# Performance work log

Hardware: AMD Instinct MI355X
Metric: run time of the kernel (lower is better)

The kernel has to match this reference:

```python
import jax, jax.numpy as jnp
import numpy as np

ITERATIONS = 3
EPS = 1e-06

def squash(s):
    # square_norm along last dim, keepdims (matches torch squash)
    sq = jnp.sum(s * s, axis=-1, keepdims=True)
    return sq / (1.0 + sq) * s / (jnp.sqrt(sq) + EPS)

def setup_inputs() -> dict:
    key = jax.random.key(0)
    k1, k2 = jax.random.split(key)
    x = jax.random.normal(k1, (64, 32, 8, 8, 16), dtype=jnp.float32)
    W = jax.random.normal(k2, (1, 32, 8, 8, 32, 16, 32), dtype=jnp.float32)
    return {"x": x, "W": W}

def reference(x, W):
    # u_hat: (B, C, H, Wd, O, D) = x (B,C,H,Wd,I) @ W (C,H,Wd,O,I,D)
    u_hat = jnp.einsum('bchwi,chwoid->bchwod', x, W[0])
    b = jnp.zeros(u_hat.shape[:-1], dtype=u_hat.dtype)  # (B,C,H,Wd,O)
    for _ in range(ITERATIONS - 1):
        c = jax.nn.softmax(b, axis=-1)
        s = jnp.sum(c[..., None] * u_hat, axis=(1, 2, 3))  # (B,O,D)
        v = squash(s)
        b = b + jnp.sum(u_hat * v[:, None, None, None], axis=-1)
    c = jax.nn.softmax(b, axis=-1)
    s = jnp.sum(c[..., None] * u_hat, axis=(1, 2, 3))
    return squash(s)  # (B, out_capsules, out_cap_dim)
```

## Files before the change

### kernel.cpp

```cpp
#include <hip/hip_runtime.h>
#include <math.h>

#define B_ 64
#define N_ 2048
#define O_ 32
#define I_ 16
#define D_ 32
#define OD_ 1024

typedef __attribute__((ext_vector_type(8))) short bf16x8;
typedef __attribute__((ext_vector_type(4))) float f32x4;

union FragU { unsigned u[4]; uint4 v; bf16x8 f; };

__device__ __forceinline__ void barrier_lds() {
  asm volatile("s_waitcnt lgkmcnt(0)\n\ts_barrier" ::: "memory");
}

template <int CTRL>
__device__ __forceinline__ float dpp_mov_f(float x) {
  return __int_as_float(
      __builtin_amdgcn_update_dpp(0, __float_as_int(x), CTRL, 0xf, 0xf, true));
}
__device__ __forceinline__ float row16_sum(float x) {
  x += dpp_mov_f<0x128>(x);
  x += dpp_mov_f<0x124>(x);
  x += dpp_mov_f<0x4e>(x);
  x += dpp_mov_f<0xb1>(x);
  return x;
}
__device__ __forceinline__ float grp32_max(float x) {
  x = fmaxf(x, dpp_mov_f<0xb1>(x));
  x = fmaxf(x, dpp_mov_f<0x4e>(x));
  x = fmaxf(x, dpp_mov_f<0x124>(x));
  x = fmaxf(x, dpp_mov_f<0x128>(x));
  x = fmaxf(x, __shfl_xor(x, 16));
  return x;
}
__device__ __forceinline__ float grp32_sum(float x) {
  x += dpp_mov_f<0xb1>(x);
  x += dpp_mov_f<0x4e>(x);
  x += dpp_mov_f<0x124>(x);
  x += dpp_mov_f<0x128>(x);
  x += __shfl_xor(x, 16);
  return x;
}

__device__ __forceinline__ void dk_split(float f, unsigned &h, unsigned &l) {
  unsigned u = __float_as_uint(f);
  h = u & 0xffff0000u;
  float lo = f - __uint_as_float(h);
  l = __float_as_uint(lo) >> 16;
}
__device__ __forceinline__ void dk_split16(float f, unsigned short &h,
                                           unsigned short &l) {
  unsigned u = __float_as_uint(f);
  unsigned hu = u & 0xffff0000u;
  h = (unsigned short)(u >> 16);
  float lo = f - __uint_as_float(hu);
  l = (unsigned short)(__float_as_uint(lo) >> 16);
}
__device__ __forceinline__ unsigned pk(unsigned short e0, unsigned short e1) {
  return (unsigned)e0 | ((unsigned)e1 << 16);
}

__global__ __launch_bounds__(256) void prep_all(const float* __restrict__ W,
                                                const float* __restrict__ x,
                                                uint4* __restrict__ WP,
                                                uint4* __restrict__ XP) {
  __shared__ float tile[8 * 512];
  const int tid = threadIdx.x;
  if (blockIdx.x < 8192) {
    const int pair0 = blockIdx.x * 8;
    const float4* gsrc = (const float4*)(W + (size_t)pair0 * 512);
    float4* lds4 = (float4*)tile;
#pragma unroll
    for (int k = 0; k < 4; ++k) lds4[tid + k * 256] = gsrc[tid + k * 256];
    __syncthreads();
    const int p = tid >> 5;
    const int d = tid & 31;
    const int pair = pair0 + p;
    unsigned short hh[I_], ll[I_];
#pragma unroll
    for (int i = 0; i < I_; ++i)
      dk_split16(tile[p * 512 + i * 32 + d], hh[i], ll[i]);
    const int c = d & 15, dhalf = d >> 4;
    size_t base = ((size_t)pair * 2 + dhalf) * 4;
#pragma unroll
    for (int sel = 0; sel < 2; ++sel) {
      const unsigned short* e = sel ? ll : hh;
#pragma unroll
      for (int qp = 0; qp < 2; ++qp) {
        uint4 u;
        u.x = pk(e[qp * 8 + 0], e[qp * 8 + 1]);
        u.y = pk(e[qp * 8 + 2], e[qp * 8 + 3]);
        u.z = pk(e[qp * 8 + 4], e[qp * 8 + 5]);
        u.w = pk(e[qp * 8 + 6], e[qp * 8 + 7]);
        WP[(base + sel * 2 + qp) * 16 + c] = u;
      }
    }
  } else {
    int t = (blockIdx.x - 8192) * 256 + tid;
    int c = t & 15, n = (t >> 4) & 2047, bg = t >> 15;
    const float4* xq =
        (const float4*)(x + ((size_t)(bg * 16 + c) * N_ + n) * I_);
    float xv[I_];
#pragma unroll
    for (int k = 0; k < 4; ++k) {
      float4 q4 = xq[k];
      xv[4 * k + 0] = q4.x;
      xv[4 * k + 1] = q4.y;
      xv[4 * k + 2] = q4.z;
      xv[4 * k + 3] = q4.w;
    }
    unsigned short hh[I_], ll[I_];
#pragma unroll
    for (int i = 0; i < I_; ++i) dk_split16(xv[i], hh[i], ll[i]);
    size_t base = ((size_t)bg * N_ + n) * 4;
#pragma unroll
    for (int sel = 0; sel < 2; ++sel) {
      const unsigned short* e = sel ? ll : hh;
#pragma unroll
      for (int qp = 0; qp < 2; ++qp) {
        uint4 u;
        u.x = pk(e[qp * 8 + 0], e[qp * 8 + 1]);
        u.y = pk(e[qp * 8 + 2], e[qp * 8 + 3]);
        u.z = pk(e[qp * 8 + 4], e[qp * 8 + 5]);
        u.w = pk(e[qp * 8 + 6], e[qp * 8 + 7]);
        XP[(base + sel * 2 + qp) * 16 + c] = u;
      }
    }
  }
}

template <int UNIFORM>
__global__ __launch_bounds__(1024, 4) void mfma_pass6(
    const uint4* __restrict__ XP, const uint4* __restrict__ WP,
    const float* __restrict__ v, float* __restrict__ partial, int NC) {
  const int tid = threadIdx.x;
  const int lane = tid & 63;
  const int w = tid >> 6;
  const int q = lane >> 4;
  const int c = lane & 15;
  const int qp = q & 1;
  const int ch = blockIdx.x;
  const int bgy = blockIdx.y;

  __shared__ uint4 xps[2][16][4][16];
  __shared__ float ls_logit[32 * O_];
  __shared__ float ls_c[32 * O_];

  const int n0 = ch * NC;

  {
    uint4* xf = (uint4*)xps;
    const int total = 2 * NC * 64;
    for (int l = tid; l < total; l += 1024) {
      int bgl = l / (NC * 64);
      int rest = l - bgl * (NC * 64);
      xf[bgl * 1024 + rest] =
          XP[(size_t)(bgy * 2 + bgl) * 131072 + (size_t)n0 * 64 + rest];
    }
  }

  f32x4 s_t[2][4];
#pragma unroll
  for (int bgl = 0; bgl < 2; ++bgl)
#pragma unroll
    for (int ct = 0; ct < 4; ++ct) s_t[bgl][ct] = (f32x4){0.f, 0.f, 0.f, 0.f};

  float vreg[2][4][4];
  if (!UNIFORM) {
#pragma unroll
    for (int bgl = 0; bgl < 2; ++bgl)
#pragma unroll
      for (int ct = 0; ct < 4; ++ct) {
        int odc = (2 * w + (ct >> 1)) * 32 + (ct & 1) * 16 + c;
#pragma unroll
        for (int r = 0; r < 4; ++r)
          vreg[bgl][ct][r] =
              v[(size_t)(bgy * 32 + bgl * 16 + q * 4 + r) * OD_ + odc];
      }
  }

  barrier_lds();

  const uint4* wbase = WP + (size_t)(2 * w) * 128 + lane;

  for (int nl = 0; nl < NC; ++nl) {
    const size_t n = (size_t)(n0 + nl);

    FragU cb[4];
#pragma unroll
    for (int ct = 0; ct < 4; ++ct) cb[ct].v = wbase[n * 4096 + ct * 64];

    if (UNIFORM) {
#pragma unroll
      for (int bgl = 0; bgl < 2; ++bgl) {
        FragU ah, al;
        ah.v = xps[bgl][nl][qp][c];
        al.v = xps[bgl][nl][2 + qp][c];
#pragma unroll
        for (int ct = 0; ct < 4; ++ct) {
          s_t[bgl][ct] = __builtin_amdgcn_mfma_f32_16x16x32_bf16(
              ah.f, cb[ct].f, s_t[bgl][ct], 0, 0, 0);
          s_t[bgl][ct] = __builtin_amdgcn_mfma_f32_16x16x32_bf16(
              al.f, cb[ct].f, s_t[bgl][ct], 0, 0, 0);
        }
      }
    } else {
      float lg[2][2][4];
#pragma unroll
      for (int bgl = 0; bgl < 2; ++bgl)
#pragma unroll
        for (int ol = 0; ol < 2; ++ol)
#pragma unroll
          for (int r = 0; r < 4; ++r) lg[bgl][ol][r] = 0.f;
#pragma unroll
      for (int bgl = 0; bgl < 2; ++bgl) {
        FragU ah, al;
        ah.v = xps[bgl][nl][qp][c];
        al.v = xps[bgl][nl][2 + qp][c];
#pragma unroll
        for (int ct = 0; ct < 4; ++ct) {
          f32x4 acc = (f32x4){0.f, 0.f, 0.f, 0.f};
          acc = __builtin_amdgcn_mfma_f32_16x16x32_bf16(ah.f, cb[ct].f, acc, 0, 0, 0);
          f32x4 u = __builtin_amdgcn_mfma_f32_16x16x32_bf16(al.f, cb[ct].f, acc, 0, 0, 0);
          int ol = ct >> 1;
#pragma unroll
          for (int r = 0; r < 4; ++r)
            lg[bgl][ol][r] = fmaf(u[r], vreg[bgl][ct][r], lg[bgl][ol][r]);
        }
      }
#pragma unroll
      for (int bgl = 0; bgl < 2; ++bgl)
#pragma unroll
        for (int ol = 0; ol < 2; ++ol)
#pragma unroll
          for (int r = 0; r < 4; ++r) lg[bgl][ol][r] = row16_sum(lg[bgl][ol][r]);
      if (c == 0) {
#pragma unroll
        for (int bgl = 0; bgl < 2; ++bgl)
#pragma unroll
          for (int ol = 0; ol < 2; ++ol)
#pragma unroll
            for (int r = 0; r < 4; ++r)
              ls_logit[(bgl * 16 + q * 4 + r) * O_ + 2 * w + ol] = lg[bgl][ol][r];
      }
      barrier_lds();
      {
        float l = ls_logit[tid];
        float mx = grp32_max(l);
        float e = __expf(l - mx);
        float sm = grp32_sum(e);
        ls_c[tid] = e / sm;
      }
      barrier_lds();
#pragma unroll
      for (int bgl = 0; bgl < 2; ++bgl) {
        FragU ah, al;
        ah.v = xps[bgl][nl][qp][c];
        al.v = xps[bgl][nl][2 + qp][c];
#pragma unroll
        for (int ct = 0; ct < 4; ++ct) {
          f32x4 acc = (f32x4){0.f, 0.f, 0.f, 0.f};
          acc = __builtin_amdgcn_mfma_f32_16x16x32_bf16(ah.f, cb[ct].f, acc, 0, 0, 0);
          f32x4 u = __builtin_amdgcn_mfma_f32_16x16x32_bf16(al.f, cb[ct].f, acc, 0, 0, 0);
          int o = 2 * w + (ct >> 1);
#pragma unroll
          for (int r = 0; r < 4; ++r) {
            float cc = ls_c[(bgl * 16 + q * 4 + r) * O_ + o];
            s_t[bgl][ct][r] = fmaf(cc, u[r], s_t[bgl][ct][r]);
          }
        }
      }
    }
  }

  const float scale = UNIFORM ? (1.f / 32.f) : 1.f;
#pragma unroll
  for (int bgl = 0; bgl < 2; ++bgl)
#pragma unroll
    for (int ct = 0; ct < 4; ++ct) {
      int odc = (2 * w + (ct >> 1)) * 32 + (ct & 1) * 16 + c;
#pragma unroll
      for (int r = 0; r < 4; ++r) {
        partial[((size_t)ch * B_ + bgy * 32 + bgl * 16 + q * 4 + r) * OD_ + odc] =
            s_t[bgl][ct][r] * scale;
      }
    }
}

template <int UNIFORM>
__global__ __launch_bounds__(512, 4) void mfma_pass_fb(
    const float* __restrict__ x, const float* __restrict__ W,
    const float* __restrict__ v, float* __restrict__ partial, int NC) {
  const int tid = threadIdx.x;
  const int lane = tid & 63;
  const int cg = tid >> 6;
  const int q = lane >> 4;
  const int c = lane & 15;
  const int ch = blockIdx.x;
  const int bg = blockIdx.y;

  __shared__ float ls_logit[16 * O_];
  __shared__ float ls_c[16 * O_];

  f32x4 s_t[8];
#pragma unroll
  for (int ct = 0; ct < 8; ++ct) s_t[ct] = (f32x4){0.f, 0.f, 0.f, 0.f};

  const int n0 = ch * NC;
  const int ih = (q & 1) * 8;
  const float* xrow = x + ((size_t)(bg * 16 + c) * N_) * I_ + ih;

  for (int nl = 0; nl < NC; ++nl) {
    const int n = n0 + nl;
    const float* xp = xrow + (size_t)n * I_;
    float4 xv0 = *(const float4*)xp;
    float4 xv1 = *(const float4*)(xp + 4);
    float xv[8] = {xv0.x, xv0.y, xv0.z, xv0.w, xv1.x, xv1.y, xv1.z, xv1.w};
    FragU a1;
#pragma unroll
    for (int p = 0; p < 4; ++p) {
      unsigned h0, l0, h1, l1;
      dk_split(xv[2 * p], h0, l0);
      dk_split(xv[2 * p + 1], h1, l1);
      a1.u[p] = (q < 2) ? ((h0 >> 16) | h1) : (l0 | (l1 << 16));
    }
    f32x4 u_t[8];
#pragma unroll
    for (int ct = 0; ct < 8; ++ct) {
      const int o = cg * 4 + (ct >> 1);
      const int d = (ct & 1) * 16 + c;
      const float* wp = W + (((size_t)n * O_ + o) * I_ + ih) * D_ + d;
      FragU b1, b2;
#pragma unroll
      for (int p = 0; p < 4; ++p) {
        unsigned h0, l0, h1, l1;
        dk_split(wp[(2 * p) * D_], h0, l0);
        dk_split(wp[(2 * p + 1) * D_], h1, l1);
        b1.u[p] = (h0 >> 16) | h1;
        b2.u[p] = l0 | (l1 << 16);
      }
      if (UNIFORM) {
        s_t[ct] = __builtin_amdgcn_mfma_f32_16x16x32_bf16(a1.f, b1.f, s_t[ct], 0, 0, 0);
        s_t[ct] = __builtin_amdgcn_mfma_f32_16x16x32_bf16(a1.f, b2.f, s_t[ct], 0, 0, 0);
      } else {
        f32x4 acc = (f32x4){0.f, 0.f, 0.f, 0.f};
        acc = __builtin_amdgcn_mfma_f32_16x16x32_bf16(a1.f, b1.f, acc, 0, 0, 0);
        u_t[ct] = __builtin_amdgcn_mfma_f32_16x16x32_bf16(a1.f, b2.f, acc, 0, 0, 0);
      }
    }
    if (!UNIFORM) {
#pragma unroll
      for (int ol = 0; ol < 4; ++ol) {
        float lg[4] = {0.f, 0.f, 0.f, 0.f};
#pragma unroll
        for (int hf = 0; hf < 2; ++hf) {
          int ct = ol * 2 + hf;
          int odc = cg * 128 + ct * 16 + c;
#pragma unroll
          for (int r = 0; r < 4; ++r)
            lg[r] = fmaf(u_t[ct][r], v[(size_t)(bg * 16 + q * 4 + r) * OD_ + odc], lg[r]);
        }
#pragma unroll
        for (int r = 0; r < 4; ++r) {
#pragma unroll
          for (int m = 1; m < 16; m <<= 1) lg[r] += __shfl_xor(lg[r], m);
        }
        if (c == 0) {
#pragma unroll
          for (int r = 0; r < 4; ++r)
            ls_logit[(q * 4 + r) * O_ + cg * 4 + ol] = lg[r];
        }
      }
      __syncthreads();
      {
        int b_l = tid >> 5, o = tid & 31;
        float l = ls_logit[b_l * O_ + o];
        float mx = l;
#pragma unroll
        for (int m = 16; m >= 1; m >>= 1) mx = fmaxf(mx, __shfl_xor(mx, m));
        float e = __expf(l - mx);
        float sm = e;
#pragma unroll
        for (int m = 16; m >= 1; m >>= 1) sm += __shfl_xor(sm, m);
        ls_c[b_l * O_ + o] = e / sm;
      }
      __syncthreads();
#pragma unroll
      for (int ol = 0; ol < 4; ++ol) {
        int o = cg * 4 + ol;
        float cc[4];
#pragma unroll
        for (int r = 0; r < 4; ++r) cc[r] = ls_c[(q * 4 + r) * O_ + o];
#pragma unroll
        for (int hf = 0; hf < 2; ++hf) {
          int ct = ol * 2 + hf;
#pragma unroll
          for (int r = 0; r < 4; ++r)
            s_t[ct][r] = fmaf(cc[r], u_t[ct][r], s_t[ct][r]);
        }
      }
    }
  }

  const float scale = UNIFORM ? (1.f / 32.f) : 1.f;
#pragma unroll
  for (int ct = 0; ct < 8; ++ct) {
#pragma unroll
    for (int r = 0; r < 4; ++r) {
      partial[((size_t)ch * B_ + bg * 16 + q * 4 + r) * OD_ + cg * 128 + ct * 16 + c] =
          s_t[ct][r] * scale;
    }
  }
}

__global__ __launch_bounds__(256) void reduce_stageA(float4* __restrict__ part,
                                                     int cq) {
  int qa = blockIdx.x >> 6;
  int g4 = (blockIdx.x & 63) * 256 + threadIdx.x;
  float4 s = make_float4(0.f, 0.f, 0.f, 0.f);
  for (int i = 0; i < cq; ++i) {
    float4 p = part[(size_t)(qa * cq + i) * 16384 + g4];
    s.x += p.x; s.y += p.y; s.z += p.z; s.w += p.w;
  }
  part[(size_t)(qa * cq) * 16384 + g4] = s;
}

__global__ __launch_bounds__(256) void reduce_stageB(
    const float4* __restrict__ part, int cq, const float4* __restrict__ prev,
    float4* __restrict__ out) {
  int g4 = blockIdx.x * 256 + threadIdx.x;
  float4 s = make_float4(0.f, 0.f, 0.f, 0.f);
#pragma unroll
  for (int qa = 0; qa < 4; ++qa) {
    float4 p = part[(size_t)(qa * cq) * 16384 + g4];
    s.x += p.x; s.y += p.y; s.z += p.z; s.w += p.w;
  }
  float sq = s.x * s.x + s.y * s.y + s.z * s.z + s.w * s.w;
#pragma unroll
  for (int m = 4; m >= 1; m >>= 1) sq += __shfl_xor(sq, m, 8);
  float scale = sq / ((1.f + sq) * (sqrtf(sq) + 1e-6f));
  float4 r = make_float4(s.x * scale, s.y * scale, s.z * scale, s.w * scale);
  if (prev) {
    float4 p = prev[g4];
    r.x += p.x; r.y += p.y; r.z += p.z; r.w += p.w;
  }
  out[g4] = r;
}

__global__ __launch_bounds__(256) void reduce_squash(
    const float4* __restrict__ part, int chunks,
    const float4* __restrict__ prev, float4* __restrict__ out) {
  int g4 = blockIdx.x * 256 + threadIdx.x;
  float4 s = make_float4(0.f, 0.f, 0.f, 0.f);
#pragma unroll 4
  for (int ch = 0; ch < chunks; ++ch) {
    float4 p = part[(size_t)ch * 16384 + g4];
    s.x += p.x; s.y += p.y; s.z += p.z; s.w += p.w;
  }
  float sq = s.x * s.x + s.y * s.y + s.z * s.z + s.w * s.w;
#pragma unroll
  for (int m = 4; m >= 1; m >>= 1) sq += __shfl_xor(sq, m, 8);
  float scale = sq / ((1.f + sq) * (sqrtf(sq) + 1e-6f));
  float4 r = make_float4(s.x * scale, s.y * scale, s.z * scale, s.w * scale);
  if (prev) {
    float4 p = prev[g4];
    r.x += p.x; r.y += p.y; r.z += p.z; r.w += p.w;
  }
  out[g4] = r;
}

extern "C" void kernel_launch(void* const* d_in, const int* in_sizes, int n_in,
                              void* d_out, int out_size, void* d_ws,
                              size_t ws_size, hipStream_t stream) {
  const float* x = (const float*)d_in[0];
  const float* W = (const float*)d_in[1];
  float* out = (float*)d_out;

  const size_t XP_FLOATS = 4ull * 2048 * 4 * 16 * 4;
  const size_t WP_FLOATS = 2048ull * 32 * 2 * 4 * 16 * 4;

  float* v1 = (float*)d_ws;
  float* vsum = v1 + 65536;
  float* partial = vsum + 65536;

  const int chunks = 128;
  bool packed_path =
      (131072 + (size_t)chunks * 65536 + XP_FLOATS + WP_FLOATS) * 4 <= ws_size;

  if (packed_path) {
    uint4* XP = (uint4*)(partial + (size_t)chunks * 65536);
    uint4* WP = XP + XP_FLOATS / 4;
    const int NC = N_ / chunks;
    const int cq = chunks / 4;
    dim3 grid(chunks, 2);

    prep_all<<<8704, 256, 0, stream>>>(W, x, WP, XP);

    mfma_pass6<1><<<grid, 1024, 0, stream>>>(XP, WP, nullptr, partial, NC);
    reduce_stageA<<<256, 256, 0, stream>>>((float4*)partial, cq);
    reduce_stageB<<<64, 256, 0, stream>>>((const float4*)partial, cq, nullptr,
                                          (float4*)v1);
    mfma_pass6<0><<<grid, 1024, 0, stream>>>(XP, WP, v1, partial, NC);
    reduce_stageA<<<256, 256, 0, stream>>>((float4*)partial, cq);
    reduce_stageB<<<64, 256, 0, stream>>>((const float4*)partial, cq,
                                          (const float4*)v1, (float4*)vsum);
    mfma_pass6<0><<<grid, 1024, 0, stream>>>(XP, WP, vsum, partial, NC);
    reduce_stageA<<<256, 256, 0, stream>>>((float4*)partial, cq);
    reduce_stageB<<<64, 256, 0, stream>>>((const float4*)partial, cq, nullptr,
                                          (float4*)out);
  } else {
    int fchunks = 128;
    while (fchunks > 1 && (131072 + (size_t)fchunks * 65536) * 4 > ws_size)
      fchunks >>= 1;
    int NC = N_ / fchunks;
    dim3 grid(fchunks, 4);

    mfma_pass_fb<1><<<grid, 512, 0, stream>>>(x, W, nullptr, partial, NC);
    reduce_squash<<<64, 256, 0, stream>>>((const float4*)partial, fchunks,
                                          nullptr, (float4*)v1);
    mfma_pass_fb<0><<<grid, 512, 0, stream>>>(x, W, v1, partial, NC);
    reduce_squash<<<64, 256, 0, stream>>>((const float4*)partial, fchunks,
                                          (const float4*)v1, (float4*)vsum);
    mfma_pass_fb<0><<<grid, 512, 0, stream>>>(x, W, vsum, partial, NC);
    reduce_squash<<<64, 256, 0, stream>>>((const float4*)partial, fchunks,
                                          nullptr, (float4*)out);
  }
}
```

Baseline: 410.9 us.

## Prefetch next W fragments, fuse two-stage reduction, nontemporal prep loads

The main MFMA pass now loads the next iteration's packed W fragments early, double-buffering them in registers so global latency overlaps with MFMA and softmax work. The logit accumulation is restructured per batch group to shrink live registers. The two reduce kernels are merged into one that splits the chunk sum across four wavefronts, combines them via LDS and then squashes, which removes a launch and an intermediate write/read. The prep kernel uses nontemporal loads for the streamed inputs. Holding the extra prefetch registers may raise register pressure.

```diff
diff --git a/kernel.cpp b/kernel.cpp
--- a/kernel.cpp
+++ b/kernel.cpp
@@ -72,10 +72,11 @@
   const int tid = threadIdx.x;
   if (blockIdx.x < 8192) {
     const int pair0 = blockIdx.x * 8;
-    const float4* gsrc = (const float4*)(W + (size_t)pair0 * 512);
-    float4* lds4 = (float4*)tile;
-#pragma unroll
-    for (int k = 0; k < 4; ++k) lds4[tid + k * 256] = gsrc[tid + k * 256];
+    const f32x4* gsrc = (const f32x4*)(W + (size_t)pair0 * 512);
+    f32x4* lds4 = (f32x4*)tile;
+#pragma unroll
+    for (int k = 0; k < 4; ++k)
+      lds4[tid + k * 256] = __builtin_nontemporal_load(gsrc + tid + k * 256);
     __syncthreads();
     const int p = tid >> 5;
     const int d = tid & 31;
@@ -102,16 +103,15 @@
   } else {
     int t = (blockIdx.x - 8192) * 256 + tid;
     int c = t & 15, n = (t >> 4) & 2047, bg = t >> 15;
-    const float4* xq =
-        (const float4*)(x + ((size_t)(bg * 16 + c) * N_ + n) * I_);
+    const f32x4* xq = (const f32x4*)(x + ((size_t)(bg * 16 + c) * N_ + n) * I_);
     float xv[I_];
 #pragma unroll
     for (int k = 0; k < 4; ++k) {
-      float4 q4 = xq[k];
-      xv[4 * k + 0] = q4.x;
-      xv[4 * k + 1] = q4.y;
-      xv[4 * k + 2] = q4.z;
-      xv[4 * k + 3] = q4.w;
+      f32x4 q4 = __builtin_nontemporal_load(xq + k);
+      xv[4 * k + 0] = q4[0];
+      xv[4 * k + 1] = q4[1];
+      xv[4 * k + 2] = q4[2];
+      xv[4 * k + 3] = q4[3];
     }
     unsigned short hh[I_], ll[I_];
 #pragma unroll
@@ -187,14 +187,19 @@
 
   const uint4* wbase = WP + (size_t)(2 * w) * 128 + lane;
 
+  FragU cb[4];
+#pragma unroll
+  for (int ct = 0; ct < 4; ++ct)
+    cb[ct].v = wbase[(size_t)n0 * 4096 + ct * 64];
+
   for (int nl = 0; nl < NC; ++nl) {
     const size_t n = (size_t)(n0 + nl);
-
-    FragU cb[4];
-#pragma unroll
-    for (int ct = 0; ct < 4; ++ct) cb[ct].v = wbase[n * 4096 + ct * 64];
+    const size_t np = (nl + 1 < NC) ? n + 1 : n;
+    FragU cbn[4];
 
     if (UNIFORM) {
+#pragma unroll
+      for (int ct = 0; ct < 4; ++ct) cbn[ct].v = wbase[np * 4096 + ct * 64];
 #pragma unroll
       for (int bgl = 0; bgl < 2; ++bgl) {
         FragU ah, al;
@@ -209,18 +214,16 @@
         }
       }
     } else {
-      float lg[2][2][4];
-#pragma unroll
-      for (int bgl = 0; bgl < 2; ++bgl)
-#pragma unroll
-        for (int ol = 0; ol < 2; ++ol)
-#pragma unroll
-          for (int r = 0; r < 4; ++r) lg[bgl][ol][r] = 0.f;
 #pragma unroll
       for (int bgl = 0; bgl < 2; ++bgl) {
         FragU ah, al;
         ah.v = xps[bgl][nl][qp][c];
         al.v = xps[bgl][nl][2 + qp][c];
+        float lg[2][4];
+#pragma unroll
+        for (int ol = 0; ol < 2; ++ol)
+#pragma unroll
+          for (int r = 0; r < 4; ++r) lg[ol][r] = 0.f;
 #pragma unroll
         for (int ct = 0; ct < 4; ++ct) {
           f32x4 acc = (f32x4){0.f, 0.f, 0.f, 0.f};
@@ -229,24 +232,23 @@
           int ol = ct >> 1;
 #pragma unroll
           for (int r = 0; r < 4; ++r)
-            lg[bgl][ol][r] = fmaf(u[r], vreg[bgl][ct][r], lg[bgl][ol][r]);
-        }
-      }
-#pragma unroll
-      for (int bgl = 0; bgl < 2; ++bgl)
+            lg[ol][r] = fmaf(u[r], vreg[bgl][ct][r], lg[ol][r]);
+        }
 #pragma unroll
         for (int ol = 0; ol < 2; ++ol)
 #pragma unroll
-          for (int r = 0; r < 4; ++r) lg[bgl][ol][r] = row16_sum(lg[bgl][ol][r]);
-      if (c == 0) {
-#pragma unroll
-        for (int bgl = 0; bgl < 2; ++bgl)
+          for (int r = 0; r < 4; ++r) lg[ol][r] = row16_sum(lg[ol][r]);
+        if (c == 0) {
 #pragma unroll
           for (int ol = 0; ol < 2; ++ol)
 #pragma unroll
             for (int r = 0; r < 4; ++r)
-              ls_logit[(bgl * 16 + q * 4 + r) * O_ + 2 * w + ol] = lg[bgl][ol][r];
-      }
+              ls_logit[(bgl * 16 + q * 4 + r) * O_ + 2 * w + ol] = lg[ol][r];
+        }
+      }
+#pragma unroll
+      for (int ct = 0; ct < 4; ++ct) cbn[ct].v = wbase[np * 4096 + ct * 64];
+
       barrier_lds();
       {
         float l = ls_logit[tid];
@@ -275,6 +277,8 @@
         }
       }
     }
+#pragma unroll
+    for (int ct = 0; ct < 4; ++ct) cb[ct] = cbn[ct];
   }
 
   const float scale = UNIFORM ? (1.f / 32.f) : 1.f;
@@ -417,38 +421,38 @@
   }
 }
 
-__global__ __launch_bounds__(256) void reduce_stageA(float4* __restrict__ part,
-                                                     int cq) {
-  int qa = blockIdx.x >> 6;
-  int g4 = (blockIdx.x & 63) * 256 + threadIdx.x;
+__global__ __launch_bounds__(256) void reduce_fused(
+    const float4* __restrict__ part, int cq4, const float4* __restrict__ prev,
+    float4* __restrict__ out) {
+  __shared__ float4 accs[4][64];
+  const int lane = threadIdx.x & 63;
+  const int cg = threadIdx.x >> 6;
+  const int g4 = blockIdx.x * 64 + lane;
   float4 s = make_float4(0.f, 0.f, 0.f, 0.f);
-  for (int i = 0; i < cq; ++i) {
-    float4 p = part[(size_t)(qa * cq + i) * 16384 + g4];
+  const int c0 = cg * cq4;
+  for (int i = 0; i < cq4; ++i) {
+    float4 p = part[(size_t)(c0 + i) * 16384 + g4];
     s.x += p.x; s.y += p.y; s.z += p.z; s.w += p.w;
   }
-  part[(size_t)(qa * cq) * 16384 + g4] = s;
-}
-
-__global__ __launch_bounds__(256) void reduce_stageB(
-    const float4* __restrict__ part, int cq, const float4* __restrict__ prev,
-    float4* __restrict__ out) {
-  int g4 = blockIdx.x * 256 + threadIdx.x;
-  float4 s = make_float4(0.f, 0.f, 0.f, 0.f);
-#pragma unroll
-  for (int qa = 0; qa < 4; ++qa) {
-    float4 p = part[(size_t)(qa * cq) * 16384 + g4];
-    s.x += p.x; s.y += p.y; s.z += p.z; s.w += p.w;
-  }
-  float sq = s.x * s.x + s.y * s.y + s.z * s.z + s.w * s.w;
-#pragma unroll
-  for (int m = 4; m >= 1; m >>= 1) sq += __shfl_xor(sq, m, 8);
-  float scale = sq / ((1.f + sq) * (sqrtf(sq) + 1e-6f));
-  float4 r = make_float4(s.x * scale, s.y * scale, s.z * scale, s.w * scale);
-  if (prev) {
-    float4 p = prev[g4];
-    r.x += p.x; r.y += p.y; r.z += p.z; r.w += p.w;
-  }
-  out[g4] = r;
+  accs[cg][lane] = s;
+  __syncthreads();
+  if (cg == 0) {
+    float4 a1 = accs[1][lane], a2 = accs[2][lane], a3 = accs[3][lane];
+    s.x += a1.x + a2.x + a3.x;
+    s.y += a1.y + a2.y + a3.y;
+    s.z += a1.z + a2.z + a3.z;
+    s.w += a1.w + a2.w + a3.w;
+    float sq = s.x * s.x + s.y * s.y + s.z * s.z + s.w * s.w;
+#pragma unroll
+    for (int m = 4; m >= 1; m >>= 1) sq += __shfl_xor(sq, m, 8);
+    float scale = sq / ((1.f + sq) * (sqrtf(sq) + 1e-6f));
+    float4 r = make_float4(s.x * scale, s.y * scale, s.z * scale, s.w * scale);
+    if (prev) {
+      float4 p = prev[g4];
+      r.x += p.x; r.y += p.y; r.z += p.z; r.w += p.w;
+    }
+    out[g4] = r;
+  }
 }
 
 __global__ __launch_bounds__(256) void reduce_squash(
@@ -495,22 +499,19 @@
     uint4* XP = (uint4*)(partial + (size_t)chunks * 65536);
     uint4* WP = XP + XP_FLOATS / 4;
     const int NC = N_ / chunks;
-    const int cq = chunks / 4;
+    const int cq4 = chunks / 4;
     dim3 grid(chunks, 2);
 
     prep_all<<<8704, 256, 0, stream>>>(W, x, WP, XP);
 
     mfma_pass6<1><<<grid, 1024, 0, stream>>>(XP, WP, nullptr, partial, NC);
-    reduce_stageA<<<256, 256, 0, stream>>>((float4*)partial, cq);
-    reduce_stageB<<<64, 256, 0, stream>>>((const float4*)partial, cq, nullptr,
+    reduce_fused<<<256, 256, 0, stream>>>((const float4*)partial, cq4, nullptr,
                                           (float4*)v1);
     mfma_pass6<0><<<grid, 1024, 0, stream>>>(XP, WP, v1, partial, NC);
-    reduce_stageA<<<256, 256, 0, stream>>>((float4*)partial, cq);
-    reduce_stageB<<<64, 256, 0, stream>>>((const float4*)partial, cq,
+    reduce_fused<<<256, 256, 0, stream>>>((const float4*)partial, cq4,
                                           (const float4*)v1, (float4*)vsum);
     mfma_pass6<0><<<grid, 1024, 0, stream>>>(XP, WP, vsum, partial, NC);
-    reduce_stageA<<<256, 256, 0, stream>>>((float4*)partial, cq);
-    reduce_stageB<<<64, 256, 0, stream>>>((const float4*)partial, cq, nullptr,
+    reduce_fused<<<256, 256, 0, stream>>>((const float4*)partial, cq4, nullptr,
                                           (float4*)out);
   } else {
     int fchunks = 128;
```

Result: faster. 377.3 us (-8.2%).
